# Optimization experiments

Hardware: AMD Instinct MI355X
Metric: run time of the kernel (lower is better)

Reference implementation:

```python
import jax, jax.numpy as jnp
import numpy as np

INV_SQRT2 = 0.7071067811865476  # ResidualLayer scale in GemNet
SILU_SCALE = 1.0 / 0.6          # ScaledSiLU scale factor


def scaled_silu(x):
    return jax.nn.silu(x) * SILU_SCALE


def setup_inputs() -> dict:
    key = jax.random.key(0)
    ks = jax.random.split(key, 9)
    E, A, D, NB = 200000, 10000, 256, 5  # edges, atoms, emb_size_edge, int_blocks+1

    def w(k, shape):
        fan_in = shape[0]
        return jax.random.normal(k, shape, jnp.float32) * (2.0 / fan_in) ** 0.5

    return {
        "x_cat": jax.random.normal(ks[0], (E, D * NB), jnp.float32),
        "edge_vec": jax.random.normal(ks[1], (E, 3), jnp.float32),
        "edge_idx": jax.random.randint(ks[2], (E,), 0, A),
        "W_in": w(ks[3], (D * NB, D)),
        "W_r1a": w(ks[4], (D, D)),
        "W_r1b": w(ks[5], (D, D)),
        "W_r2a": w(ks[6], (D, D)),
        "W_r2b": w(ks[7], (D, D)),
        "W_out": w(ks[8], (D, 1)),
        "n_atoms": A,
    }


def reference(x_cat, edge_vec, edge_idx, W_in, W_r1a, W_r1b, W_r2a, W_r2b, W_out, n_atoms):
    # out_mlp_F: Dense(in->emb) + 2 residual layers (all Dense are bias-free + ScaledSiLU)
    x = scaled_silu(x_cat @ W_in)                                   # [E, D]
    x = (x + scaled_silu(scaled_silu(x @ W_r1a) @ W_r1b)) * INV_SQRT2
    x = (x + scaled_silu(scaled_silu(x @ W_r2a) @ W_r2b)) * INV_SQRT2
    # out_forces: Dense(D -> 1, bias=False, no activation)
    F_st = x @ W_out                                                # [E, 1]
    # F_st_vec = F_st[:, :, None] * edge_vec[:, None, :] -> squeeze the size-1 dim
    F_vec = F_st * edge_vec                                         # [E, 3]
    # scatter_add over target atom index
    forces = jax.ops.segment_sum(F_vec, edge_idx, num_segments=n_atoms)  # [A, 3]
    return forces
```

## Files before the change

kernel.cpp:

```cpp
#include <hip/hip_runtime.h>

typedef __attribute__((ext_vector_type(4))) float f32x4;
typedef __attribute__((ext_vector_type(8))) __bf16 bf16x8;
typedef __attribute__((ext_vector_type(8))) unsigned short us8;
typedef __attribute__((ext_vector_type(4))) unsigned short us4;
typedef unsigned short u16;

#define SSILU_SCALE (1.0f / 0.6f)
#define INV_SQRT2 0.70710678118654752f

__device__ __forceinline__ u16 f2bf(float f) {
    __bf16 h = (__bf16)f;
    return __builtin_bit_cast(u16, h);
}
__device__ __forceinline__ float bf2f(u16 h) {
    union { unsigned int u; float f; } v; v.u = ((unsigned int)h) << 16;
    return v.f;
}
__device__ __forceinline__ float silu_(float x) {
    float e = __expf(-x);
    float s = __builtin_amdgcn_rcpf(1.0f + e);
    return x * s;
}

__global__ __launch_bounds__(256) void prep_kernel(
    const float* __restrict__ Win, const float* __restrict__ W1a,
    const float* __restrict__ W1b, const float* __restrict__ W2a,
    const float* __restrict__ W2b, u16* __restrict__ WinF,
    u16* __restrict__ Wfrag, float* __restrict__ out, int outN) {
    int i = blockIdx.x * 256 + threadIdx.x;
    if (i < 327680) {
        int e = i & 7, lane = (i >> 3) & 63, n = (i >> 9) & 3;
        int kk = (i >> 11) & 1, w = (i >> 12) & 3, kt = i >> 14;
        int lo = lane & 15, hi = lane >> 4;
        int k = kt * 64 + kk * 32 + hi * 8 + e;
        int col = w * 64 + n * 16 + lo;
        WinF[i] = f2bf(Win[k * 256 + col]);
        return;
    }
    int j = i - 327680;
    if (j < 262144) {
        int g = j >> 16, r = j & 65535;
        int chunk = r >> 9, within = r & 511;
        int lane = within >> 3, e = within & 7;
        int w = chunk >> 5, kk = (chunk >> 2) & 7, n = chunk & 3;
        int lo = lane & 15, hi = lane >> 4;
        int col = w * 64 + n * 16 + lo;
        int k = kk * 32 + hi * 8 + e;
        const float* W = (g == 0) ? W1a : (g == 1) ? W1b : (g == 2) ? W2a : W2b;
        Wfrag[j] = f2bf(W[k * 256 + col] * SSILU_SCALE);
        return;
    }
    int z = j - 262144;
    if (z < outN) out[z] = 0.0f;
}

__global__ __launch_bounds__(256, 2) void fused_kernel(
    const float* __restrict__ A, const u16* __restrict__ WinF,
    const u16* __restrict__ Wfrag, const float* __restrict__ Wout,
    const float* __restrict__ evec, const int* __restrict__ eidx,
    float* __restrict__ out) {
    __shared__ u16 xb[64 * 256];
    __shared__ u16 tb[64 * 256];
    __shared__ float fpart[4][64];
    const int t = threadIdx.x, w = t >> 6, l = t & 63;
    const int lo = l & 15, hi = l >> 4;
    const int swz = (lo & 7) << 4;
    const long rowbase = (long)blockIdx.x * 64;
    char* xbB = (char*)xb;
    char* tbB = (char*)tb;
    char* As0 = tbB;
    char* As1 = tbB + 16384;

    f32x4 acc[4][4];
#pragma unroll
    for (int m = 0; m < 4; m++)
#pragma unroll
        for (int n = 0; n < 4; n++) acc[m][n] = (f32x4){0.f, 0.f, 0.f, 0.f};

    auto RUNOFF = [&](int m, int n) {
        int row = m * 16 + lo;
        int colb = (w * 64 + n * 16 + hi * 4) * 2;
        return row * 512 + (colb ^ ((row & 7) << 4));
    };

    float4 va0[4][2], va1[4][2];
    auto LOADA = [&](int kb, float4 (&va)[4][2]) {
#pragma unroll
        for (int c = 0; c < 4; ++c) {
            int idx = t + c * 256;
            int r = idx >> 4, k8 = (idx & 15) * 8;
            const float* s = A + (rowbase + r) * 1280 + kb + k8;
            va[c][0] = *(const float4*)s;
            va[c][1] = *(const float4*)(s + 4);
        }
    };
    auto WRITEA = [&](char* dst, const float4 (&va)[4][2]) {
#pragma unroll
        for (int c = 0; c < 4; ++c) {
            int idx = t + c * 256;
            int r = idx >> 4, k8 = (idx & 15) * 8;
            us8 p;
            p[0] = f2bf(va[c][0].x); p[1] = f2bf(va[c][0].y);
            p[2] = f2bf(va[c][0].z); p[3] = f2bf(va[c][0].w);
            p[4] = f2bf(va[c][1].x); p[5] = f2bf(va[c][1].y);
            p[6] = f2bf(va[c][1].z); p[7] = f2bf(va[c][1].w);
            *(us8*)(dst + r * 256 + ((k8 * 2) ^ ((r & 7) << 4))) = p;
        }
    };
    const u16* WinFw = WinF + w * 4096 + l * 8;
    auto LOADB = [&](int kt, bf16x8 (&b)[8]) {
        const u16* base = WinFw + kt * 16384;
#pragma unroll
        for (int kkL = 0; kkL < 2; ++kkL)
#pragma unroll
            for (int n = 0; n < 4; ++n)
                b[kkL * 4 + n] = __builtin_bit_cast(bf16x8,
                    *(const us8*)(base + kkL * 2048 + n * 512));
    };
    auto MFMA_HALF = [&](const char* AB, int half, const bf16x8 (&b)[8]) {
#pragma unroll
        for (int kkL = 0; kkL < 2; ++kkL) {
            int kbyte = (half * 2 + kkL) * 64 + hi * 16;
            bf16x8 af[4];
#pragma unroll
            for (int m = 0; m < 4; m++) {
                int r = m * 16 + lo;
                af[m] = __builtin_bit_cast(bf16x8,
                    *(const us8*)(AB + r * 256 + (kbyte ^ swz)));
            }
#pragma unroll
            for (int m = 0; m < 4; m++)
#pragma unroll
                for (int n = 0; n < 4; n++)
                    acc[m][n] = __builtin_amdgcn_mfma_f32_16x16x32_bf16(
                        b[kkL * 4 + n], af[m], acc[m][n], 0, 0, 0);
        }
    };
    auto FENCE = [&]() {
        asm volatile("s_waitcnt lgkmcnt(0)" ::: "memory");
        __builtin_amdgcn_sched_barrier(0);
        __builtin_amdgcn_s_barrier();
    };

    {
        bf16x8 bc[8], bn[8];

        LOADA(0, va0);
        WRITEA(As0, va0);
        LOADB(0, bc);
        LOADA(128, va1);
        FENCE();

        auto STEP = [&](int s, const char* AScur, char* ASnxt,
                        const float4 (&vaCons)[4][2], float4 (&vaFill)[4][2]) {
            const bool more = (s < 9);
            if (s <= 7) LOADA((s + 2) * 128, vaFill);
            LOADB(2 * s + 1, bn);
            __builtin_amdgcn_sched_barrier(0);
            MFMA_HALF(AScur, 0, bc);
            if (more) LOADB(2 * s + 2, bc);
            MFMA_HALF(AScur, 1, bn);
            if (more) WRITEA(ASnxt, vaCons);
            FENCE();
        };

        for (int i = 0; i < 5; ++i) {
            STEP(2 * i,     As0, As1, va1, va0);
            STEP(2 * i + 1, As1, As0, va0, va1);
        }
    }

#pragma unroll
    for (int m = 0; m < 4; m++)
#pragma unroll
        for (int n = 0; n < 4; n++) {
            us4 p;
#pragma unroll
            for (int j = 0; j < 4; j++) p[j] = f2bf(silu_(acc[m][n][j]));
            *(us4*)(xbB + RUNOFF(m, n)) = p;
        }

    const u16* Wfw = Wfrag + w * 16384;
    bf16x8 b0[4], b1[4], b2[4];

    auto LW = [&](const u16* Wg, int kk, bf16x8 (&b)[4]) {
        const u16* base = Wg + kk * 2048 + l * 8;
#pragma unroll
        for (int n = 0; n < 4; ++n)
            b[n] = __builtin_bit_cast(bf16x8, *(const us8*)(base + n * 512));
    };
    auto GEMM = [&](const char* AB, const u16* Wg) {
#pragma unroll
        for (int m = 0; m < 4; m++)
#pragma unroll
            for (int n = 0; n < 4; n++) acc[m][n] = (f32x4){0.f, 0.f, 0.f, 0.f};
#pragma unroll
        for (int kk = 0; kk < 8; ++kk) {
            if (kk < 6) {
                const int s = (kk + 2) % 3;
                if (s == 0)      LW(Wg, kk + 2, b0);
                else if (s == 1) LW(Wg, kk + 2, b1);
                else             LW(Wg, kk + 2, b2);
            }
            int kbyte = kk * 64 + hi * 16;
            bf16x8 af[4];
#pragma unroll
            for (int m = 0; m < 4; m++) {
                int r = m * 16 + lo;
                af[m] = __builtin_bit_cast(bf16x8,
                    *(const us8*)(AB + r * 512 + (kbyte ^ ((r & 7) << 4))));
            }
            const bf16x8 (&bu)[4] = (kk % 3 == 0) ? b0 : (kk % 3 == 1) ? b1 : b2;
#pragma unroll
            for (int m = 0; m < 4; m++)
#pragma unroll
                for (int n = 0; n < 4; n++)
                    acc[m][n] = __builtin_amdgcn_mfma_f32_16x16x32_bf16(
                        bu[n], af[m], acc[m][n], 0, 0, 0);
        }
    };

    LW(Wfw + 0 * 65536, 0, b0);
    LW(Wfw + 0 * 65536, 1, b1);
    FENCE();
    GEMM(xbB, Wfw + 0 * 65536);
#pragma unroll
    for (int m = 0; m < 4; m++)
#pragma unroll
        for (int n = 0; n < 4; n++) {
            us4 p;
#pragma unroll
            for (int j = 0; j < 4; j++) p[j] = f2bf(silu_(acc[m][n][j]));
            *(us4*)(tbB + RUNOFF(m, n)) = p;
        }
    LW(Wfw + 1 * 65536, 0, b0);
    LW(Wfw + 1 * 65536, 1, b1);
    FENCE();

    GEMM(tbB, Wfw + 1 * 65536);
#pragma unroll
    for (int m = 0; m < 4; m++)
#pragma unroll
        for (int n = 0; n < 4; n++) {
            char* p = xbB + RUNOFF(m, n);
            us4 xv = *(const us4*)p;
            us4 o;
#pragma unroll
            for (int j = 0; j < 4; j++)
                o[j] = f2bf((bf2f(xv[j]) + silu_(acc[m][n][j])) * INV_SQRT2);
            *(us4*)p = o;
        }
    LW(Wfw + 2 * 65536, 0, b0);
    LW(Wfw + 2 * 65536, 1, b1);
    FENCE();

    GEMM(xbB, Wfw + 2 * 65536);
#pragma unroll
    for (int m = 0; m < 4; m++)
#pragma unroll
        for (int n = 0; n < 4; n++) {
            us4 p;
#pragma unroll
            for (int j = 0; j < 4; j++) p[j] = f2bf(silu_(acc[m][n][j]));
            *(us4*)(tbB + RUNOFF(m, n)) = p;
        }
    LW(Wfw + 3 * 65536, 0, b0);
    LW(Wfw + 3 * 65536, 1, b1);
    FENCE();

    GEMM(tbB, Wfw + 3 * 65536);
    float wo2[4][4];
#pragma unroll
    for (int n = 0; n < 4; n++)
#pragma unroll
        for (int j = 0; j < 4; j++)
            wo2[n][j] = Wout[w * 64 + n * 16 + hi * 4 + j] * SSILU_SCALE;

    float part[4];
#pragma unroll
    for (int m = 0; m < 4; m++) part[m] = 0.f;
#pragma unroll
    for (int m = 0; m < 4; m++)
#pragma unroll
        for (int n = 0; n < 4; n++) {
            const char* p = xbB + RUNOFF(m, n);
            us4 xv = *(const us4*)p;
#pragma unroll
            for (int j = 0; j < 4; j++) {
                float xf = (bf2f(xv[j]) + silu_(acc[m][n][j])) * INV_SQRT2;
                part[m] += xf * wo2[n][j];
            }
        }
#pragma unroll
    for (int m = 0; m < 4; m++) {
        float v = part[m];
        v += __shfl_xor(v, 16);
        v += __shfl_xor(v, 32);
        if (hi == 0) fpart[w][m * 16 + lo] = v;
    }
    __syncthreads();

    if (t < 64) {
        int r = t;
        float F = fpart[0][r] + fpart[1][r] + fpart[2][r] + fpart[3][r];
        long e = rowbase + r;
        float vx = evec[e * 3 + 0], vy = evec[e * 3 + 1], vz = evec[e * 3 + 2];
        int a = eidx[e];
        atomicAdd(&out[a * 3 + 0], F * vx);
        atomicAdd(&out[a * 3 + 1], F * vy);
        atomicAdd(&out[a * 3 + 2], F * vz);
    }
}

extern "C" void kernel_launch(void* const* d_in, const int* in_sizes, int n_in,
                              void* d_out, int out_size, void* d_ws, size_t ws_size,
                              hipStream_t stream) {
    const float* x_cat = (const float*)d_in[0];
    const float* evec  = (const float*)d_in[1];
    const int*   eidx  = (const int*)d_in[2];
    const float* Win   = (const float*)d_in[3];
    const float* W1a   = (const float*)d_in[4];
    const float* W1b   = (const float*)d_in[5];
    const float* W2a   = (const float*)d_in[6];
    const float* W2b   = (const float*)d_in[7];
    const float* Wout  = (const float*)d_in[8];
    float* out = (float*)d_out;
    const int E = in_sizes[1] / 3;

    u16* WinF  = (u16*)d_ws;
    u16* Wfrag = WinF + 327680;

    int prepN = 327680 + 262144 + out_size;
    prep_kernel<<<(prepN + 255) / 256, 256, 0, stream>>>(
        Win, W1a, W1b, W2a, W2b, WinF, Wfrag, out, out_size);
    fused_kernel<<<E / 64, 256, 0, stream>>>(
        x_cat, WinF, Wfrag, Wout, evec, eidx, out);
}
```

Baseline: 355.6 us.

## Double block tile to 128 rows with 8 waves sharing weight fragments

Grows each workgroup from 64 to 128 edge rows and 4 to 8 waves. The two halves of the block each take 64 rows and share the same column split. The aim is to amortise per-block setup, barriers and the scatter epilogue over more rows. In exchange, shared memory per block roughly doubles, to about 130KB, which likely cuts blocks per CU from 2 to 1. Bounds checks are added for a partial last tile.

```diff
diff --git a/kernel.cpp b/kernel.cpp
--- a/kernel.cpp
+++ b/kernel.cpp
@@ -55,22 +55,23 @@
     if (z < outN) out[z] = 0.0f;
 }
 
-__global__ __launch_bounds__(256, 2) void fused_kernel(
+__global__ __launch_bounds__(512, 2) void fused_kernel(
     const float* __restrict__ A, const u16* __restrict__ WinF,
     const u16* __restrict__ Wfrag, const float* __restrict__ Wout,
     const float* __restrict__ evec, const int* __restrict__ eidx,
-    float* __restrict__ out) {
-    __shared__ u16 xb[64 * 256];
-    __shared__ u16 tb[64 * 256];
-    __shared__ float fpart[4][64];
+    float* __restrict__ out, int E) {
+    __shared__ u16 xb[128 * 256];
+    __shared__ u16 tb[128 * 256];
+    __shared__ float fpart[4][128];
     const int t = threadIdx.x, w = t >> 6, l = t & 63;
+    const int hh = w >> 2, wq = w & 3;
     const int lo = l & 15, hi = l >> 4;
     const int swz = (lo & 7) << 4;
-    const long rowbase = (long)blockIdx.x * 64;
+    const long rowbase = (long)blockIdx.x * 128;
     char* xbB = (char*)xb;
     char* tbB = (char*)tb;
     char* As0 = tbB;
-    char* As1 = tbB + 16384;
+    char* As1 = tbB + 32768;
 
     f32x4 acc[4][4];
 #pragma unroll
@@ -79,8 +80,8 @@
         for (int n = 0; n < 4; n++) acc[m][n] = (f32x4){0.f, 0.f, 0.f, 0.f};
 
     auto RUNOFF = [&](int m, int n) {
-        int row = m * 16 + lo;
-        int colb = (w * 64 + n * 16 + hi * 4) * 2;
+        int row = hh * 64 + m * 16 + lo;
+        int colb = (wq * 64 + n * 16 + hi * 4) * 2;
         return row * 512 + (colb ^ ((row & 7) << 4));
     };
 
@@ -88,9 +89,11 @@
     auto LOADA = [&](int kb, float4 (&va)[4][2]) {
 #pragma unroll
         for (int c = 0; c < 4; ++c) {
-            int idx = t + c * 256;
+            int idx = t + c * 512;
             int r = idx >> 4, k8 = (idx & 15) * 8;
-            const float* s = A + (rowbase + r) * 1280 + kb + k8;
+            long gr = rowbase + r;
+            if (gr >= E) gr = E - 1;
+            const float* s = A + gr * 1280 + kb + k8;
             va[c][0] = *(const float4*)s;
             va[c][1] = *(const float4*)(s + 4);
         }
@@ -98,7 +101,7 @@
     auto WRITEA = [&](char* dst, const float4 (&va)[4][2]) {
 #pragma unroll
         for (int c = 0; c < 4; ++c) {
-            int idx = t + c * 256;
+            int idx = t + c * 512;
             int r = idx >> 4, k8 = (idx & 15) * 8;
             us8 p;
             p[0] = f2bf(va[c][0].x); p[1] = f2bf(va[c][0].y);
@@ -108,7 +111,7 @@
             *(us8*)(dst + r * 256 + ((k8 * 2) ^ ((r & 7) << 4))) = p;
         }
     };
-    const u16* WinFw = WinF + w * 4096 + l * 8;
+    const u16* WinFw = WinF + wq * 4096 + l * 8;
     auto LOADB = [&](int kt, bf16x8 (&b)[8]) {
         const u16* base = WinFw + kt * 16384;
 #pragma unroll
@@ -118,14 +121,14 @@
                 b[kkL * 4 + n] = __builtin_bit_cast(bf16x8,
                     *(const us8*)(base + kkL * 2048 + n * 512));
     };
-    auto MFMA_HALF = [&](const char* AB, int half, const bf16x8 (&b)[8]) {
+    auto MFMA_HALF = [&](const char* AB, int kh, const bf16x8 (&b)[8]) {
 #pragma unroll
         for (int kkL = 0; kkL < 2; ++kkL) {
-            int kbyte = (half * 2 + kkL) * 64 + hi * 16;
+            int kbyte = (kh * 2 + kkL) * 64 + hi * 16;
             bf16x8 af[4];
 #pragma unroll
             for (int m = 0; m < 4; m++) {
-                int r = m * 16 + lo;
+                int r = hh * 64 + m * 16 + lo;
                 af[m] = __builtin_bit_cast(bf16x8,
                     *(const us8*)(AB + r * 256 + (kbyte ^ swz)));
             }
@@ -181,7 +184,7 @@
             *(us4*)(xbB + RUNOFF(m, n)) = p;
         }
 
-    const u16* Wfw = Wfrag + w * 16384;
+    const u16* Wfw = Wfrag + wq * 16384;
     bf16x8 b0[4], b1[4], b2[4];
 
     auto LW = [&](const u16* Wg, int kk, bf16x8 (&b)[4]) {
@@ -207,7 +210,7 @@
             bf16x8 af[4];
 #pragma unroll
             for (int m = 0; m < 4; m++) {
-                int r = m * 16 + lo;
+                int r = hh * 64 + m * 16 + lo;
                 af[m] = __builtin_bit_cast(bf16x8,
                     *(const us8*)(AB + r * 512 + (kbyte ^ ((r & 7) << 4))));
             }
@@ -275,7 +278,7 @@
     for (int n = 0; n < 4; n++)
 #pragma unroll
         for (int j = 0; j < 4; j++)
-            wo2[n][j] = Wout[w * 64 + n * 16 + hi * 4 + j] * SSILU_SCALE;
+            wo2[n][j] = Wout[wq * 64 + n * 16 + hi * 4 + j] * SSILU_SCALE;
 
     float part[4];
 #pragma unroll
@@ -297,19 +300,21 @@
         float v = part[m];
         v += __shfl_xor(v, 16);
         v += __shfl_xor(v, 32);
-        if (hi == 0) fpart[w][m * 16 + lo] = v;
+        if (hi == 0) fpart[wq][hh * 64 + m * 16 + lo] = v;
     }
     __syncthreads();
 
-    if (t < 64) {
+    if (t < 128) {
         int r = t;
-        float F = fpart[0][r] + fpart[1][r] + fpart[2][r] + fpart[3][r];
         long e = rowbase + r;
-        float vx = evec[e * 3 + 0], vy = evec[e * 3 + 1], vz = evec[e * 3 + 2];
-        int a = eidx[e];
-        atomicAdd(&out[a * 3 + 0], F * vx);
-        atomicAdd(&out[a * 3 + 1], F * vy);
-        atomicAdd(&out[a * 3 + 2], F * vz);
+        if (e < E) {
+            float F = fpart[0][r] + fpart[1][r] + fpart[2][r] + fpart[3][r];
+            float vx = evec[e * 3 + 0], vy = evec[e * 3 + 1], vz = evec[e * 3 + 2];
+            int a = eidx[e];
+            atomicAdd(&out[a * 3 + 0], F * vx);
+            atomicAdd(&out[a * 3 + 1], F * vy);
+            atomicAdd(&out[a * 3 + 2], F * vz);
+        }
     }
 }
 
@@ -334,6 +339,6 @@
     int prepN = 327680 + 262144 + out_size;
     prep_kernel<<<(prepN + 255) / 256, 256, 0, stream>>>(
         Win, W1a, W1b, W2a, W2b, WinF, Wfrag, out, out_size);
-    fused_kernel<<<E / 64, 256, 0, stream>>>(
-        x_cat, WinF, Wfrag, Wout, evec, eidx, out);
-}
+    fused_kernel<<<(E + 127) / 128, 512, 0, stream>>>(
+        x_cat, WinF, Wfrag, Wout, evec, eidx, out, E);
+}
```

New measurement: 405.1 us. +13.9%, slower.
